# Kernel optimization log

Hardware: AMD Instinct MI355X
Metric: run time of the kernel (lower is better)

## Reference

```python
import jax, jax.numpy as jnp
import numpy as np

B, N, T, D, H, O = 4, 40, 100, 4, 128, 2
E = N * (N - 1)
BN_EPS = 1e-5


def setup_inputs() -> dict:
    ks = jax.random.split(jax.random.key(0), 32)
    def rn(i, shape, s=0.1):
        return jax.random.normal(ks[i], shape, dtype=jnp.float32) * s
    # fully-connected off-diagonal edge list -> one-hot rel matrices (NRI convention)
    off = np.ones((N, N), dtype=np.float32) - np.eye(N, dtype=np.float32)
    r, c = np.where(off > 0)
    eye = np.eye(N, dtype=np.float32)
    return {
        "inputs": jax.random.normal(ks[0], (B, N, T, D), dtype=jnp.float32),
        "rel_rec": jnp.asarray(eye[r]),
        "rel_send": jnp.asarray(eye[c]),
        "conv1_w": rn(1, (H, 2 * D, 5)), "conv1_b": rn(2, (H,)),
        "bn1_g": jnp.ones((H,), jnp.float32), "bn1_b": jnp.zeros((H,), jnp.float32),
        "bn1_m": rn(3, (H,), 0.05), "bn1_v": 1.0 + jnp.abs(rn(4, (H,), 0.05)),
        "conv2_w": rn(5, (H, H, 5)), "conv2_b": rn(6, (H,)),
        "bn2_g": jnp.ones((H,), jnp.float32), "bn2_b": jnp.zeros((H,), jnp.float32),
        "bn2_m": rn(7, (H,), 0.05), "bn2_v": 1.0 + jnp.abs(rn(8, (H,), 0.05)),
        "convp_w": rn(9, (H, H, 1)), "convp_b": rn(10, (H,)),
        "conva_w": rn(11, (1, H, 1)), "conva_b": rn(12, (1,)),
        "mlp1_w1": rn(13, (H, H)), "mlp1_b1": rn(14, (H,)),
        "mlp1_w2": rn(15, (H, H)), "mlp1_b2": rn(16, (H,)),
        "mlp2_w1": rn(17, (H, H)), "mlp2_b1": rn(18, (H,)),
        "mlp2_w2": rn(19, (H, H)), "mlp2_b2": rn(20, (H,)),
        "mlp3_w1": rn(21, (3 * H, H)), "mlp3_b1": rn(22, (H,)),
        "mlp3_w2": rn(23, (H, H)), "mlp3_b2": rn(24, (H,)),
        "fco_w": rn(25, (H, O)), "fco_b": rn(26, (O,)),
    }


def _conv1d(x, w, b):
    # x: [n, Cin, T], w: [Cout, Cin, K] (torch layout), VALID padding, stride 1
    y = jax.lax.conv_general_dilated(x, w, (1,), "VALID", dimension_numbers=("NCH", "OIH", "NCH"))
    return y + b[None, :, None]


def _bn(x, g, b, m, v):
    # eval-mode BatchNorm1d over channel axis 1
    return (x - m[None, :, None]) * jax.lax.rsqrt(v[None, :, None] + BN_EPS) * g[None, :, None] + b[None, :, None]


def _mlp(x, w1, b1, w2, b2):
    # NRI MLP with no_bn=True, dropout off (eval)
    h = jax.nn.elu(x @ w1 + b1)
    return jax.nn.elu(h @ w2 + b2)


def _forward(inputs, rel_rec, rel_send, p):
    # node2edge_temporal: [B,N,T,D] -> [B*E, 2D, T] (senders then receivers)
    xf = inputs.reshape(B, N, T * D)
    recv = jnp.einsum("en,bnf->bef", rel_rec, xf).reshape(B * E, T, D).transpose(0, 2, 1)
    send = jnp.einsum("en,bnf->bef", rel_send, xf).reshape(B * E, T, D).transpose(0, 2, 1)
    x = jnp.concatenate([send, recv], axis=1)
    # CNN over time (eval mode)
    x = _bn(jax.nn.relu(_conv1d(x, p["conv1_w"], p["conv1_b"])), p["bn1_g"], p["bn1_b"], p["bn1_m"], p["bn1_v"])
    n, c, t = x.shape
    x = x.reshape(n, c, t // 2, 2).max(axis=-1)  # MaxPool1d(kernel=2, stride=2)
    x = _bn(jax.nn.relu(_conv1d(x, p["conv2_w"], p["conv2_b"])), p["bn2_g"], p["bn2_b"], p["bn2_m"], p["bn2_v"])
    pred = _conv1d(x, p["convp_w"], p["convp_b"])
    attn = jax.nn.softmax(_conv1d(x, p["conva_w"], p["conva_b"]), axis=2)
    x = (pred * attn).mean(axis=2).reshape(B, E, H)  # attention-weighted temporal pooling
    x = _mlp(x, p["mlp1_w1"], p["mlp1_b1"], p["mlp1_w2"], p["mlp1_b2"])
    x_skip = x
    # edge2node: mean-aggregate incoming edges per node (divide by incoming.size(1)=N)
    inc = jnp.einsum("en,beh->bnh", rel_rec, x) / N
    x = _mlp(inc, p["mlp2_w1"], p["mlp2_b1"], p["mlp2_w2"], p["mlp2_b2"])
    # node2edge: cat(senders, receivers) on feature dim
    sn = jnp.einsum("en,bnh->beh", rel_send, x)
    rc = jnp.einsum("en,bnh->beh", rel_rec, x)
    x = jnp.concatenate([sn, rc, x_skip], axis=2)
    x = _mlp(x, p["mlp3_w1"], p["mlp3_b1"], p["mlp3_w2"], p["mlp3_b2"])
    return x @ p["fco_w"] + p["fco_b"]


def reference(inputs, rel_rec, rel_send, conv1_w, conv1_b, bn1_g, bn1_b, bn1_m, bn1_v, conv2_w, conv2_b, bn2_g, bn2_b, bn2_m, bn2_v, convp_w, convp_b, conva_w, conva_b, mlp1_w1, mlp1_b1, mlp1_w2, mlp1_b2, mlp2_w1, mlp2_b1, mlp2_w2, mlp2_b2, mlp3_w1, mlp3_b1, mlp3_w2, mlp3_b2, fco_w, fco_b):
    args = dict(locals())
    p = {k: v for k, v in args.items() if k not in ("inputs", "rel_rec", "rel_send")}
    return _forward(inputs, rel_rec, rel_send, p)
```

## Files before the change

kernel.cpp:

```cpp
#include <hip/hip_runtime.h>

#define E_CNT 1560
#define B_CNT 4
#define N_CNT 40
#define T_CNT 100

typedef __attribute__((ext_vector_type(8))) short bf16x8;
typedef __attribute__((ext_vector_type(4))) float f32x4;

__device__ __forceinline__ short f2bf(float f) {
  union { float f; unsigned u; } v; v.f = f;
  unsigned r = v.u + 0x7FFFu + ((v.u >> 16) & 1u);
  return (short)(r >> 16);
}
__device__ __forceinline__ float bf2f(short s) {
  union { unsigned u; float f; } v; v.u = ((unsigned)(unsigned short)s) << 16;
  return v.f;
}
__device__ __forceinline__ int cvtpk(float lo, float hi) {
  int r;
  asm("v_cvt_pk_bf16_f32 %0, %1, %2" : "=v"(r) : "v"(lo), "v"(hi));
  return r;
}
__device__ __forceinline__ float eluf(float x) { return x > 0.f ? x : (__expf(x) - 1.f); }
__device__ __forceinline__ f32x4 mfma16(bf16x8 a, bf16x8 b, f32x4 c) {
  return __builtin_amdgcn_mfma_f32_16x16x32_bf16(a, b, c, 0, 0, 0);
}
__device__ __forceinline__ int swz(int row, int bytecol) {
  return row * 256 + (bytecol ^ ((row & 7) << 4));
}

enum : size_t {
  OFF_A1   = 0,
  OFF_A2   = OFF_A1 + 16384,
  OFF_INPB = OFF_A2 + 163840,
  OFF_B1F  = OFF_INPB + 128000,
  OFF_O1   = OFF_B1F + 512,
  OFF_B2F  = OFF_O1 + 512,
  OFF_O2   = OFF_B2F + 512,
  OFF_BC1  = OFF_O2 + 512,
  OFF_W1T1 = OFF_BC1 + 512,
  OFF_W1T2 = OFF_W1T1 + 32768,
  OFF_W3T1 = OFF_W1T2 + 32768,
  OFF_W3T2 = OFF_W3T1 + 98304,
  OFF_RIDX = OFF_W3T2 + 32768,
  OFF_SIDX = OFF_RIDX + 6400,
  OFF_EF   = OFF_SIDX + 6400,
  OFF_XSK  = OFF_EF + 1597440,
  OFF_XN   = OFF_XSK + 1597440,
  WS_NEED  = OFF_XN + 40960
};

__global__ void k_prep(
    const float* __restrict__ inp,
    const float* __restrict__ c1w, const float* __restrict__ c1b,
    const float* __restrict__ c2w, const float* __restrict__ c2b,
    const float* __restrict__ cpw, const float* __restrict__ cpb,
    const float* __restrict__ g1, const float* __restrict__ be1, const float* __restrict__ m1, const float* __restrict__ v1,
    const float* __restrict__ g2, const float* __restrict__ be2, const float* __restrict__ m2, const float* __restrict__ v2,
    const float* __restrict__ m1w1, const float* __restrict__ m1b1, const float* __restrict__ m1w2,
    const float* __restrict__ m3w1, const float* __restrict__ m3w2,
    const float* __restrict__ relr, const float* __restrict__ rels,
    short* __restrict__ A1, short* __restrict__ A2, short* __restrict__ inpb,
    float* __restrict__ b1f, float* __restrict__ o1, float* __restrict__ b2f, float* __restrict__ o2,
    float* __restrict__ bc1,
    short* __restrict__ w1t1, short* __restrict__ w1t2, short* __restrict__ w3t1, short* __restrict__ w3t2,
    int* __restrict__ ridx, int* __restrict__ sidx)
{
  const int id = blockIdx.x * blockDim.x + threadIdx.x;
  const int NTH = gridDim.x * blockDim.x;
  for (int i = id; i < 8192; i += NTH) {
    int co = i >> 6, col = i & 63, k = col >> 3, c = col & 7;
    float sa = g1[co] * rsqrtf(v1[co] + 1e-5f);
    A1[i] = (k < 5) ? f2bf(c1w[co * 40 + c * 5 + k] * sa) : (short)0;
  }
  for (int i = id; i < 81920; i += NTH) {
    int s = i >> 14, rem = i & 16383, co = rem >> 7, ci = rem & 127;
    float sb = g2[co] * rsqrtf(v2[co] + 1e-5f);
    A2[i] = f2bf(c2w[(co * 128 + ci) * 5 + s] * sb);
  }
  for (int i = id; i < 64000; i += NTH) inpb[i] = f2bf(inp[i]);
  for (int i = id; i < 128; i += NTH) {
    float sa = g1[i] * rsqrtf(v1[i] + 1e-5f);
    b1f[i] = c1b[i] * sa; o1[i] = be1[i] - m1[i] * sa;
    float sb = g2[i] * rsqrtf(v2[i] + 1e-5f);
    b2f[i] = c2b[i] * sb; o2[i] = be2[i] - m2[i] * sb;
  }
  for (int idx = id; idx < 16384; idx += NTH) {
    int c = idx >> 7, i = idx & 127;
    float s = 0.f;
    for (int o = 0; o < 128; ++o) s += cpw[o * 128 + i] * m1w1[o * 128 + c];
    w1t1[idx] = f2bf(s);
  }
  for (int c = id; c < 128; c += NTH) {
    float s = 0.f;
    for (int o = 0; o < 128; ++o) s += cpb[o] * m1w1[o * 128 + c];
    bc1[c] = m1b1[c] + s * (1.0f / 44.0f);
  }
  for (int i = id; i < 16384; i += NTH) {
    int co = i >> 7, k = i & 127;
    w1t2[i] = f2bf(m1w2[k * 128 + co]);
    w3t2[i] = f2bf(m3w2[k * 128 + co]);
  }
  for (int i = id; i < 49152; i += NTH) {
    int co = i / 384, k = i - co * 384;
    w3t1[i] = f2bf(m3w1[k * 128 + co]);
  }
  for (int i = id; i < E_CNT; i += NTH) {
    int rr = 0, ss = 0;
    for (int n = 0; n < N_CNT; ++n) {
      if (relr[i * N_CNT + n] > 0.5f) rr = n;
      if (rels[i * N_CNT + n] > 0.5f) ss = n;
    }
    ridx[i] = rr; sidx[i] = ss;
  }
}

__global__ __launch_bounds__(256, 5) void k_cnn(
    const short* __restrict__ inpb,
    const short* __restrict__ A1, const short* __restrict__ A2,
    const float* __restrict__ b1fv, const float* __restrict__ o1v,
    const float* __restrict__ b2fv, const float* __restrict__ o2v,
    const float* __restrict__ wa,
    const int* __restrict__ ridx, const int* __restrict__ sidx,
    short* __restrict__ ef)
{
  __shared__ short h1t[2][52 * 128];
  __shared__ short rawb[4 * 408];
  __shared__ float lgp[2][4][48];
  __shared__ float attnS[2][48];

  const int tid = threadIdx.x;
  const int lane = tid & 63;
  const int w = tid >> 6;
  const int g = lane >> 4;
  const int lr = lane & 15;

  const int eg0 = blockIdx.x * 2;
  const int b = eg0 / E_CNT;
  const int e0 = eg0 - b * E_CNT;
  const short* nbase = inpb + (size_t)b * N_CNT * 400;

  if (tid < 200) {
    int row = tid / 50, off = (tid % 50) * 8;
    int e = row >> 1;
    int node = (row & 1) ? ridx[e0 + e] : sidx[e0 + e];
    *(bf16x8*)&rawb[row * 408 + off] = *(const bf16x8*)(nbase + node * 400 + off);
  }
  {
    int ee = tid >> 7, off = (tid & 127) * 4;
    *(short4*)&h1t[ee][48 * 128 + off] = make_short4(0, 0, 0, 0);
  }
  __syncthreads();

  {
    bf16x8 a1f[2][2];
#pragma unroll
    for (int ks = 0; ks < 2; ++ks)
#pragma unroll
      for (int m = 0; m < 2; ++m)
        a1f[ks][m] = *(const bf16x8*)(A1 + (32 * w + 16 * m + lr) * 64 + ks * 32 + 8 * g);
    f32x4 bc[2], oc[2];
#pragma unroll
    for (int m = 0; m < 2; ++m) {
      int rb = 32 * w + 16 * m + 4 * g;
      bc[m] = *(const f32x4*)(b1fv + rb);
      oc[m] = *(const f32x4*)(o1v + rb);
    }
#pragma unroll
    for (int e = 0; e < 2; ++e) {
#pragma unroll
      for (int n = 0; n < 6; ++n) {
        f32x4 acc[2];
        acc[0] = f32x4{0.f, 0.f, 0.f, 0.f};
        acc[1] = f32x4{0.f, 0.f, 0.f, 0.f};
#pragma unroll
        for (int ks = 0; ks < 2; ++ks) {
          int tc = n * 16 + lr + 4 * ks + g;
          tc = tc > 99 ? 99 : tc;
          union { bf16x8 v; int2 h[2]; } u;
          u.h[0] = *(const int2*)&rawb[(2 * e) * 408 + tc * 4];
          u.h[1] = *(const int2*)&rawb[(2 * e + 1) * 408 + tc * 4];
#pragma unroll
          for (int m = 0; m < 2; ++m) acc[m] = mfma16(a1f[ks][m], u.v, acc[m]);
        }
#pragma unroll
        for (int m = 0; m < 2; ++m) {
          int rb = 32 * w + 16 * m + 4 * g;
          float p[4];
#pragma unroll
          for (int r = 0; r < 4; ++r) {
            float v = fmaxf(acc[m][r] + bc[m][r], 0.f) + oc[m][r];
            float o = __shfl_xor(v, 1);
            p[r] = fmaxf(v, o);
          }
          int lo = cvtpk(p[0], p[1]), hi = cvtpk(p[2], p[3]);
          if ((lane & 1) == 0) {
            int t = 8 * n + (lr >> 1);
            *(int2*)((char*)h1t[e] + swz(t, rb * 2)) = make_int2(lo, hi);
          }
        }
      }
    }
  }
  __syncthreads();

  f32x4 acc[2][2][3];
#pragma unroll
  for (int e = 0; e < 2; ++e)
#pragma unroll
    for (int m = 0; m < 2; ++m)
#pragma unroll
      for (int n = 0; n < 3; ++n) acc[e][m][n] = f32x4{0.f, 0.f, 0.f, 0.f};
  {
    const short* a2b = A2 + (32 * w + lr) * 128 + 8 * g;
    const int c0 = 16 * g;
#pragma unroll
    for (int sh = 0; sh < 5; ++sh) {
      const int rowb = (lr + sh) * 256;
      const int xr = ((lr + sh) & 7) << 4;
#pragma unroll
      for (int ks = 0; ks < 4; ++ks) {
        bf16x8 af0 = *(const bf16x8*)(a2b + sh * 16384 + ks * 32);
        bf16x8 af1 = *(const bf16x8*)(a2b + sh * 16384 + 16 * 128 + ks * 32);
        const char* p0 = (const char*)h1t[0] + (rowb + ((ks * 64 + c0) ^ xr));
#pragma unroll
        for (int e = 0; e < 2; ++e) {
          const char* pe = p0 + e * 13312;
#pragma unroll
          for (int n = 0; n < 3; ++n) {
            bf16x8 bfr = *(const bf16x8*)(pe + n * 4096);
            acc[e][0][n] = mfma16(af0, bfr, acc[e][0][n]);
            acc[e][1][n] = mfma16(af1, bfr, acc[e][1][n]);
          }
        }
      }
    }
  }

  {
    f32x4 bc2[2], oc2[2], wam[2];
#pragma unroll
    for (int m = 0; m < 2; ++m) {
      int rb = 32 * w + 16 * m + 4 * g;
      bc2[m] = *(const f32x4*)(b2fv + rb);
      oc2[m] = *(const f32x4*)(o2v + rb);
      wam[m] = *(const f32x4*)(wa + rb);
    }
#pragma unroll
    for (int e = 0; e < 2; ++e)
#pragma unroll
      for (int n = 0; n < 3; ++n) {
        float p = 0.f;
#pragma unroll
        for (int m = 0; m < 2; ++m) {
#pragma unroll
          for (int r = 0; r < 4; ++r) {
            float v = fmaxf(acc[e][m][n][r] + bc2[m][r], 0.f) + oc2[m][r];
            acc[e][m][n][r] = v;
            p += wam[m][r] * v;
          }
        }
        p += __shfl_xor(p, 16);
        p += __shfl_xor(p, 32);
        if (g == 0) lgp[e][w][n * 16 + lr] = p;
      }
  }
  __syncthreads();

  if (w < 2) {
    int ee = w;
    float x = -3e38f;
    if (lane < 44) x = lgp[ee][0][lane] + lgp[ee][1][lane] + lgp[ee][2][lane] + lgp[ee][3][lane];
    float mx = x;
#pragma unroll
    for (int d = 32; d; d >>= 1) mx = fmaxf(mx, __shfl_xor(mx, d));
    float ex = (lane < 44) ? __expf(x - mx) : 0.f;
    float sm = ex;
#pragma unroll
    for (int d = 32; d; d >>= 1) sm += __shfl_xor(sm, d);
    if (lane < 48) attnS[ee][lane] = (lane < 44) ? ex / (sm * 44.f) : 0.f;
  }
  __syncthreads();

#pragma unroll
  for (int e = 0; e < 2; ++e)
#pragma unroll
    for (int m = 0; m < 2; ++m) {
      f32x4 red = f32x4{0.f, 0.f, 0.f, 0.f};
#pragma unroll
      for (int n = 0; n < 3; ++n) {
        float aw = attnS[e][n * 16 + lr];
        red += acc[e][m][n] * aw;
      }
      float p[4];
#pragma unroll
      for (int r = 0; r < 4; ++r) {
        float q = red[r];
        q += __shfl_xor(q, 1);
        q += __shfl_xor(q, 2);
        q += __shfl_xor(q, 4);
        q += __shfl_xor(q, 8);
        p[r] = q;
      }
      int lo = cvtpk(p[0], p[1]), hi = cvtpk(p[2], p[3]);
      if (lr == 0)
        *(int2*)(ef + (size_t)(eg0 + e) * 128 + 32 * w + 16 * m + 4 * g) = make_int2(lo, hi);
    }
}

__global__ __launch_bounds__(256, 2) void k_mlp1(
    const short* __restrict__ ef,
    const short* __restrict__ w1t, const float* __restrict__ b1,
    const short* __restrict__ w2t, const float* __restrict__ b2,
    short* __restrict__ xskip)
{
  __shared__ short hbuf[16 * 136];
  __shared__ short obuf[16 * 128];
  const int tid = threadIdx.x, lane = tid & 63, w = tid >> 6, g = lane >> 4, lr = lane & 15;
  const int mbase = blockIdx.x * 16;

  f32x4 acc[2];
  acc[0] = f32x4{0.f, 0.f, 0.f, 0.f};
  acc[1] = f32x4{0.f, 0.f, 0.f, 0.f};
#pragma unroll
  for (int ks = 0; ks < 4; ++ks) {
    bf16x8 afr = *(const bf16x8*)(ef + (size_t)(mbase + lr) * 128 + ks * 32 + 8 * g);
#pragma unroll
    for (int ni = 0; ni < 2; ++ni) {
      int co = (2 * w + ni) * 16 + lr;
      bf16x8 bfr = *(const bf16x8*)(w1t + co * 128 + ks * 32 + 8 * g);
      acc[ni] = mfma16(afr, bfr, acc[ni]);
    }
  }
#pragma unroll
  for (int ni = 0; ni < 2; ++ni) {
    int co = (2 * w + ni) * 16 + lr;
    float bias = b1[co];
#pragma unroll
    for (int r = 0; r < 4; ++r) hbuf[(4 * g + r) * 136 + co] = f2bf(eluf(acc[ni][r] + bias));
  }
  __syncthreads();
  acc[0] = f32x4{0.f, 0.f, 0.f, 0.f};
  acc[1] = f32x4{0.f, 0.f, 0.f, 0.f};
#pragma unroll
  for (int ks = 0; ks < 4; ++ks) {
    bf16x8 afr = *(const bf16x8*)&hbuf[lr * 136 + ks * 32 + 8 * g];
#pragma unroll
    for (int ni = 0; ni < 2; ++ni) {
      int co = (2 * w + ni) * 16 + lr;
      bf16x8 bfr = *(const bf16x8*)(w2t + co * 128 + ks * 32 + 8 * g);
      acc[ni] = mfma16(afr, bfr, acc[ni]);
    }
  }
#pragma unroll
  for (int ni = 0; ni < 2; ++ni) {
    int co = (2 * w + ni) * 16 + lr;
    float bias = b2[co];
#pragma unroll
    for (int r = 0; r < 4; ++r) obuf[(4 * g + r) * 128 + co] = f2bf(eluf(acc[ni][r] + bias));
  }
  __syncthreads();
  *(bf16x8*)(xskip + (size_t)mbase * 128 + tid * 8) = *(const bf16x8*)&obuf[tid * 8];
}

__global__ __launch_bounds__(128, 4) void k_node(
    const short* __restrict__ xskip, const int* __restrict__ ridx,
    const float* __restrict__ w1, const float* __restrict__ b1,
    const float* __restrict__ w2, const float* __restrict__ b2,
    short* __restrict__ xn)
{
  __shared__ float incs[128];
  __shared__ float hb[128];
  __shared__ int lst[64];
  __shared__ int lcnt;
  const int tid = threadIdx.x;
  const int bn_ = blockIdx.x;
  const int b = bn_ / N_CNT, n = bn_ - b * N_CNT;
  if (tid == 0) lcnt = 0;
  __syncthreads();
  for (int e2 = tid; e2 < E_CNT; e2 += 128) {
    if (ridx[e2] == n) {
      int p = atomicAdd(&lcnt, 1);
      if (p < 64) lst[p] = e2;
    }
  }
  __syncthreads();
  const int m_ = lcnt < 64 ? lcnt : 64;
  const short* base = xskip + (size_t)b * E_CNT * 128 + tid;
  float acc = 0.f;
  for (int i = 0; i < m_; ++i) acc += bf2f(base[(size_t)lst[i] * 128]);
  incs[tid] = acc * 0.025f;
  __syncthreads();
  float h = b1[tid];
  for (int k = 0; k < 128; ++k) h += incs[k] * w1[k * 128 + tid];
  hb[tid] = eluf(h);
  __syncthreads();
  float h2 = b2[tid];
  for (int k = 0; k < 128; ++k) h2 += hb[k] * w2[k * 128 + tid];
  xn[(size_t)bn_ * 128 + tid] = f2bf(eluf(h2));
}

__global__ __launch_bounds__(256, 2) void k_final(
    const short* __restrict__ xn, const short* __restrict__ xskip,
    const int* __restrict__ ridx, const int* __restrict__ sidx,
    const short* __restrict__ w1t, const float* __restrict__ b1,
    const short* __restrict__ w2t, const float* __restrict__ b2,
    const float* __restrict__ fcw, const float* __restrict__ fcb,
    float* __restrict__ out)
{
  __shared__ short hbuf[16 * 136];
  __shared__ short h2buf[16 * 136];
  const int tid = threadIdx.x, lane = tid & 63, w = tid >> 6, g = lane >> 4, lr = lane & 15;
  const int mbase = blockIdx.x * 16;
  const int row = mbase + lr;
  const int b = row / E_CNT;
  const int e = row - b * E_CNT;
  const short* aS = xn + (size_t)(b * N_CNT + sidx[e]) * 128;
  const short* aR = xn + (size_t)(b * N_CNT + ridx[e]) * 128;
  const short* aK = xskip + (size_t)row * 128;

  f32x4 acc[2];
  acc[0] = f32x4{0.f, 0.f, 0.f, 0.f};
  acc[1] = f32x4{0.f, 0.f, 0.f, 0.f};
#pragma unroll
  for (int ks = 0; ks < 12; ++ks) {
    int k = ks * 32 + 8 * g;
    const short* ap = (k < 128) ? (aS + k) : (k < 256) ? (aR + (k - 128)) : (aK + (k - 256));
    bf16x8 afr = *(const bf16x8*)ap;
#pragma unroll
    for (int ni = 0; ni < 2; ++ni) {
      int co = (2 * w + ni) * 16 + lr;
      bf16x8 bfr = *(const bf16x8*)(w1t + co * 384 + ks * 32 + 8 * g);
      acc[ni] = mfma16(afr, bfr, acc[ni]);
    }
  }
#pragma unroll
  for (int ni = 0; ni < 2; ++ni) {
    int co = (2 * w + ni) * 16 + lr;
    float bias = b1[co];
#pragma unroll
    for (int r = 0; r < 4; ++r) hbuf[(4 * g + r) * 136 + co] = f2bf(eluf(acc[ni][r] + bias));
  }
  __syncthreads();
  acc[0] = f32x4{0.f, 0.f, 0.f, 0.f};
  acc[1] = f32x4{0.f, 0.f, 0.f, 0.f};
#pragma unroll
  for (int ks = 0; ks < 4; ++ks) {
    bf16x8 afr = *(const bf16x8*)&hbuf[lr * 136 + ks * 32 + 8 * g];
#pragma unroll
    for (int ni = 0; ni < 2; ++ni) {
      int co = (2 * w + ni) * 16 + lr;
      bf16x8 bfr = *(const bf16x8*)(w2t + co * 128 + ks * 32 + 8 * g);
      acc[ni] = mfma16(afr, bfr, acc[ni]);
    }
  }
#pragma unroll
  for (int ni = 0; ni < 2; ++ni) {
    int co = (2 * w + ni) * 16 + lr;
    float bias = b2[co];
#pragma unroll
    for (int r = 0; r < 4; ++r) h2buf[(4 * g + r) * 136 + co] = f2bf(eluf(acc[ni][r] + bias));
  }
  __syncthreads();
  if (tid < 32) {
    int e2 = tid >> 1, o = tid & 1;
    float s = fcb[o];
    for (int k = 0; k < 128; ++k) s += bf2f(h2buf[e2 * 136 + k]) * fcw[k * 2 + o];
    out[(size_t)(mbase + e2) * 2 + o] = s;
  }
}

extern "C" void kernel_launch(void* const* d_in, const int* in_sizes, int n_in,
                              void* d_out, int out_size, void* d_ws, size_t ws_size,
                              hipStream_t stream) {
  (void)in_sizes; (void)n_in; (void)out_size; (void)ws_size;
  const float* inp  = (const float*)d_in[0];
  const float* relr = (const float*)d_in[1];
  const float* rels = (const float*)d_in[2];
  const float* c1w  = (const float*)d_in[3];
  const float* c1b  = (const float*)d_in[4];
  const float* g1   = (const float*)d_in[5];
  const float* be1  = (const float*)d_in[6];
  const float* m1   = (const float*)d_in[7];
  const float* v1   = (const float*)d_in[8];
  const float* c2w  = (const float*)d_in[9];
  const float* c2b  = (const float*)d_in[10];
  const float* g2   = (const float*)d_in[11];
  const float* be2  = (const float*)d_in[12];
  const float* m2   = (const float*)d_in[13];
  const float* v2   = (const float*)d_in[14];
  const float* cpw  = (const float*)d_in[15];
  const float* cpb  = (const float*)d_in[16];
  const float* caw  = (const float*)d_in[17];
  const float* m1w1 = (const float*)d_in[19];
  const float* m1b1 = (const float*)d_in[20];
  const float* m1w2 = (const float*)d_in[21];
  const float* m1b2 = (const float*)d_in[22];
  const float* m2w1 = (const float*)d_in[23];
  const float* m2b1 = (const float*)d_in[24];
  const float* m2w2 = (const float*)d_in[25];
  const float* m2b2 = (const float*)d_in[26];
  const float* m3w1 = (const float*)d_in[27];
  const float* m3b1 = (const float*)d_in[28];
  const float* m3w2 = (const float*)d_in[29];
  const float* m3b2 = (const float*)d_in[30];
  const float* fcw  = (const float*)d_in[31];
  const float* fcb  = (const float*)d_in[32];
  float* out = (float*)d_out;

  char* ws = (char*)d_ws;
  short* A1   = (short*)(ws + OFF_A1);
  short* A2   = (short*)(ws + OFF_A2);
  short* inpb = (short*)(ws + OFF_INPB);
  float* b1f  = (float*)(ws + OFF_B1F);
  float* o1   = (float*)(ws + OFF_O1);
  float* b2f  = (float*)(ws + OFF_B2F);
  float* o2   = (float*)(ws + OFF_O2);
  float* bc1  = (float*)(ws + OFF_BC1);
  short* w1t1 = (short*)(ws + OFF_W1T1);
  short* w1t2 = (short*)(ws + OFF_W1T2);
  short* w3t1 = (short*)(ws + OFF_W3T1);
  short* w3t2 = (short*)(ws + OFF_W3T2);
  int*   ridx = (int*)(ws + OFF_RIDX);
  int*   sidx = (int*)(ws + OFF_SIDX);
  short* ef   = (short*)(ws + OFF_EF);
  short* xsk  = (short*)(ws + OFF_XSK);
  short* xn   = (short*)(ws + OFF_XN);

  k_prep<<<256, 256, 0, stream>>>(inp, c1w, c1b, c2w, c2b, cpw, cpb,
                                  g1, be1, m1, v1, g2, be2, m2, v2,
                                  m1w1, m1b1, m1w2, m3w1, m3w2, relr, rels,
                                  A1, A2, inpb, b1f, o1, b2f, o2, bc1,
                                  w1t1, w1t2, w3t1, w3t2, ridx, sidx);
  k_cnn<<<B_CNT * E_CNT / 2, 256, 0, stream>>>(inpb, A1, A2, b1f, o1, b2f, o2,
                                               caw, ridx, sidx, ef);
  k_mlp1<<<390, 256, 0, stream>>>(ef, w1t1, bc1, w1t2, m1b2, xsk);
  k_node<<<B_CNT * N_CNT, 128, 0, stream>>>(xsk, ridx, m2w1, m2b1, m2w2, m2b2, xn);
  k_final<<<390, 256, 0, stream>>>(xn, xsk, ridx, sidx, w3t1, m3b1, w3t2, m3b2, fcw, fcb, out);
}
```

Measured before the change: 127.3 us.

## Split CNN kernel work across 8 waves, one edge per wave group

The CNN kernel now launches 512 threads per block instead of 256, assigning each group of four waves to one of the two edges rather than having every wave loop over both edges. This halves the per-wave accumulator count and the per-wave MFMA chain, which cuts register pressure and adds more waves to hide latency. In exchange, each wave reloads the A1/A2 weight fragments for its own edge, so weight loads per block double. The larger block may also reduce the number of resident blocks per CU.

```diff
diff --git a/kernel.cpp b/kernel.cpp
--- a/kernel.cpp
+++ b/kernel.cpp
@@ -116,7 +116,7 @@
   }
 }
 
-__global__ __launch_bounds__(256, 5) void k_cnn(
+__global__ __launch_bounds__(512, 8) void k_cnn(
     const short* __restrict__ inpb,
     const short* __restrict__ A1, const short* __restrict__ A2,
     const float* __restrict__ b1fv, const float* __restrict__ o1v,
@@ -135,6 +135,8 @@
   const int w = tid >> 6;
   const int g = lane >> 4;
   const int lr = lane & 15;
+  const int e = w >> 2;
+  const int q = w & 3;
 
   const int eg0 = blockIdx.x * 2;
   const int b = eg0 / E_CNT;
@@ -143,14 +145,11 @@
 
   if (tid < 200) {
     int row = tid / 50, off = (tid % 50) * 8;
-    int e = row >> 1;
-    int node = (row & 1) ? ridx[e0 + e] : sidx[e0 + e];
+    int ee = row >> 1;
+    int node = (row & 1) ? ridx[e0 + ee] : sidx[e0 + ee];
     *(bf16x8*)&rawb[row * 408 + off] = *(const bf16x8*)(nbase + node * 400 + off);
   }
-  {
-    int ee = tid >> 7, off = (tid & 127) * 4;
-    *(short4*)&h1t[ee][48 * 128 + off] = make_short4(0, 0, 0, 0);
-  }
+  ((int*)h1t[tid >> 8])[3072 + (tid & 255)] = 0;
   __syncthreads();
 
   {
@@ -159,61 +158,57 @@
     for (int ks = 0; ks < 2; ++ks)
 #pragma unroll
       for (int m = 0; m < 2; ++m)
-        a1f[ks][m] = *(const bf16x8*)(A1 + (32 * w + 16 * m + lr) * 64 + ks * 32 + 8 * g);
+        a1f[ks][m] = *(const bf16x8*)(A1 + (32 * q + 16 * m + lr) * 64 + ks * 32 + 8 * g);
     f32x4 bc[2], oc[2];
 #pragma unroll
     for (int m = 0; m < 2; ++m) {
-      int rb = 32 * w + 16 * m + 4 * g;
+      int rb = 32 * q + 16 * m + 4 * g;
       bc[m] = *(const f32x4*)(b1fv + rb);
       oc[m] = *(const f32x4*)(o1v + rb);
     }
 #pragma unroll
-    for (int e = 0; e < 2; ++e) {
-#pragma unroll
-      for (int n = 0; n < 6; ++n) {
-        f32x4 acc[2];
-        acc[0] = f32x4{0.f, 0.f, 0.f, 0.f};
-        acc[1] = f32x4{0.f, 0.f, 0.f, 0.f};
-#pragma unroll
-        for (int ks = 0; ks < 2; ++ks) {
-          int tc = n * 16 + lr + 4 * ks + g;
-          tc = tc > 99 ? 99 : tc;
-          union { bf16x8 v; int2 h[2]; } u;
-          u.h[0] = *(const int2*)&rawb[(2 * e) * 408 + tc * 4];
-          u.h[1] = *(const int2*)&rawb[(2 * e + 1) * 408 + tc * 4];
-#pragma unroll
-          for (int m = 0; m < 2; ++m) acc[m] = mfma16(a1f[ks][m], u.v, acc[m]);
+    for (int n = 0; n < 6; ++n) {
+      f32x4 acc1[2];
+      acc1[0] = f32x4{0.f, 0.f, 0.f, 0.f};
+      acc1[1] = f32x4{0.f, 0.f, 0.f, 0.f};
+#pragma unroll
+      for (int ks = 0; ks < 2; ++ks) {
+        int tc = n * 16 + lr + 4 * ks + g;
+        tc = tc > 99 ? 99 : tc;
+        union { bf16x8 v; int2 h[2]; } u;
+        u.h[0] = *(const int2*)&rawb[(2 * e) * 408 + tc * 4];
+        u.h[1] = *(const int2*)&rawb[(2 * e + 1) * 408 + tc * 4];
+#pragma unroll
+        for (int m = 0; m < 2; ++m) acc1[m] = mfma16(a1f[ks][m], u.v, acc1[m]);
+      }
+#pragma unroll
+      for (int m = 0; m < 2; ++m) {
+        int rb = 32 * q + 16 * m + 4 * g;
+        float p[4];
+#pragma unroll
+        for (int r = 0; r < 4; ++r) {
+          float v = fmaxf(acc1[m][r] + bc[m][r], 0.f) + oc[m][r];
+          float o = __shfl_xor(v, 1);
+          p[r] = fmaxf(v, o);
         }
-#pragma unroll
-        for (int m = 0; m < 2; ++m) {
-          int rb = 32 * w + 16 * m + 4 * g;
-          float p[4];
-#pragma unroll
-          for (int r = 0; r < 4; ++r) {
-            float v = fmaxf(acc[m][r] + bc[m][r], 0.f) + oc[m][r];
-            float o = __shfl_xor(v, 1);
-            p[r] = fmaxf(v, o);
-          }
-          int lo = cvtpk(p[0], p[1]), hi = cvtpk(p[2], p[3]);
-          if ((lane & 1) == 0) {
-            int t = 8 * n + (lr >> 1);
-            *(int2*)((char*)h1t[e] + swz(t, rb * 2)) = make_int2(lo, hi);
-          }
+        int lo = cvtpk(p[0], p[1]), hi = cvtpk(p[2], p[3]);
+        if ((lane & 1) == 0) {
+          int t = 8 * n + (lr >> 1);
+          *(int2*)((char*)h1t[e] + swz(t, rb * 2)) = make_int2(lo, hi);
         }
       }
     }
   }
   __syncthreads();
 
-  f32x4 acc[2][2][3];
-#pragma unroll
-  for (int e = 0; e < 2; ++e)
-#pragma unroll
-    for (int m = 0; m < 2; ++m)
-#pragma unroll
-      for (int n = 0; n < 3; ++n) acc[e][m][n] = f32x4{0.f, 0.f, 0.f, 0.f};
+  f32x4 acc[2][3];
+#pragma unroll
+  for (int m = 0; m < 2; ++m)
+#pragma unroll
+    for (int n = 0; n < 3; ++n) acc[m][n] = f32x4{0.f, 0.f, 0.f, 0.f};
   {
-    const short* a2b = A2 + (32 * w + lr) * 128 + 8 * g;
+    const short* a2b = A2 + (32 * q + lr) * 128 + 8 * g;
+    const char* hb = (const char*)h1t[e];
     const int c0 = 16 * g;
 #pragma unroll
     for (int sh = 0; sh < 5; ++sh) {
@@ -223,16 +218,12 @@
       for (int ks = 0; ks < 4; ++ks) {
         bf16x8 af0 = *(const bf16x8*)(a2b + sh * 16384 + ks * 32);
         bf16x8 af1 = *(const bf16x8*)(a2b + sh * 16384 + 16 * 128 + ks * 32);
-        const char* p0 = (const char*)h1t[0] + (rowb + ((ks * 64 + c0) ^ xr));
-#pragma unroll
-        for (int e = 0; e < 2; ++e) {
-          const char* pe = p0 + e * 13312;
-#pragma unroll
-          for (int n = 0; n < 3; ++n) {
-            bf16x8 bfr = *(const bf16x8*)(pe + n * 4096);
-            acc[e][0][n] = mfma16(af0, bfr, acc[e][0][n]);
-            acc[e][1][n] = mfma16(af1, bfr, acc[e][1][n]);
-          }
+        const char* p0 = hb + (rowb + ((ks * 64 + c0) ^ xr));
+#pragma unroll
+        for (int n = 0; n < 3; ++n) {
+          bf16x8 bfr = *(const bf16x8*)(p0 + n * 4096);
+          acc[0][n] = mfma16(af0, bfr, acc[0][n]);
+          acc[1][n] = mfma16(af1, bfr, acc[1][n]);
         }
       }
     }
@@ -242,29 +233,27 @@
     f32x4 bc2[2], oc2[2], wam[2];
 #pragma unroll
     for (int m = 0; m < 2; ++m) {
-      int rb = 32 * w + 16 * m + 4 * g;
+      int rb = 32 * q + 16 * m + 4 * g;
       bc2[m] = *(const f32x4*)(b2fv + rb);
       oc2[m] = *(const f32x4*)(o2v + rb);
       wam[m] = *(const f32x4*)(wa + rb);
     }
 #pragma unroll
-    for (int e = 0; e < 2; ++e)
-#pragma unroll
-      for (int n = 0; n < 3; ++n) {
-        float p = 0.f;
-#pragma unroll
-        for (int m = 0; m < 2; ++m) {
-#pragma unroll
-          for (int r = 0; r < 4; ++r) {
-            float v = fmaxf(acc[e][m][n][r] + bc2[m][r], 0.f) + oc2[m][r];
-            acc[e][m][n][r] = v;
-            p += wam[m][r] * v;
-          }
+    for (int n = 0; n < 3; ++n) {
+      float p = 0.f;
+#pragma unroll
+      for (int m = 0; m < 2; ++m) {
+#pragma unroll
+        for (int r = 0; r < 4; ++r) {
+          float v = fmaxf(acc[m][n][r] + bc2[m][r], 0.f) + oc2[m][r];
+          acc[m][n][r] = v;
+          p += wam[m][r] * v;
         }
-        p += __shfl_xor(p, 16);
-        p += __shfl_xor(p, 32);
-        if (g == 0) lgp[e][w][n * 16 + lr] = p;
       }
+      p += __shfl_xor(p, 16);
+      p += __shfl_xor(p, 32);
+      if (g == 0) lgp[e][q][n * 16 + lr] = p;
+    }
   }
   __syncthreads();
 
@@ -284,29 +273,27 @@
   __syncthreads();
 
 #pragma unroll
-  for (int e = 0; e < 2; ++e)
-#pragma unroll
-    for (int m = 0; m < 2; ++m) {
-      f32x4 red = f32x4{0.f, 0.f, 0.f, 0.f};
-#pragma unroll
-      for (int n = 0; n < 3; ++n) {
-        float aw = attnS[e][n * 16 + lr];
-        red += acc[e][m][n] * aw;
-      }
-      float p[4];
-#pragma unroll
-      for (int r = 0; r < 4; ++r) {
-        float q = red[r];
-        q += __shfl_xor(q, 1);
-        q += __shfl_xor(q, 2);
-        q += __shfl_xor(q, 4);
-        q += __shfl_xor(q, 8);
-        p[r] = q;
-      }
-      int lo = cvtpk(p[0], p[1]), hi = cvtpk(p[2], p[3]);
-      if (lr == 0)
-        *(int2*)(ef + (size_t)(eg0 + e) * 128 + 32 * w + 16 * m + 4 * g) = make_int2(lo, hi);
-    }
+  for (int m = 0; m < 2; ++m) {
+    f32x4 red = f32x4{0.f, 0.f, 0.f, 0.f};
+#pragma unroll
+    for (int n = 0; n < 3; ++n) {
+      float aw = attnS[e][n * 16 + lr];
+      red += acc[m][n] * aw;
+    }
+    float p[4];
+#pragma unroll
+    for (int r = 0; r < 4; ++r) {
+      float s = red[r];
+      s += __shfl_xor(s, 1);
+      s += __shfl_xor(s, 2);
+      s += __shfl_xor(s, 4);
+      s += __shfl_xor(s, 8);
+      p[r] = s;
+    }
+    int lo = cvtpk(p[0], p[1]), hi = cvtpk(p[2], p[3]);
+    if (lr == 0)
+      *(int2*)(ef + (size_t)(eg0 + e) * 128 + 32 * q + 16 * m + 4 * g) = make_int2(lo, hi);
+  }
 }
 
 __global__ __launch_bounds__(256, 2) void k_mlp1(
@@ -533,7 +520,7 @@
                                   m1w1, m1b1, m1w2, m3w1, m3w2, relr, rels,
                                   A1, A2, inpb, b1f, o1, b2f, o2, bc1,
                                   w1t1, w1t2, w3t1, w3t2, ridx, sidx);
-  k_cnn<<<B_CNT * E_CNT / 2, 256, 0, stream>>>(inpb, A1, A2, b1f, o1, b2f, o2,
+  k_cnn<<<B_CNT * E_CNT / 2, 512, 0, stream>>>(inpb, A1, A2, b1f, o1, b2f, o2,
                                                caw, ridx, sidx, ef);
   k_mlp1<<<390, 256, 0, stream>>>(ef, w1t1, bc1, w1t2, m1b2, xsk);
   k_node<<<B_CNT * N_CNT, 128, 0, stream>>>(xsk, ridx, m2w1, m2b1, m2w2, m2b2, xn);
```

Measured after the change: 181.6 us. 42.6% more time.

## Fuse edge MLP1 into the CNN kernel epilogue via shared memory

Applied to the files above, without the earlier changes.

Removes the separate k_mlp1 launch. The k_cnn kernel now keeps its pooled edge features in shared memory, reusing the h1t buffer with a swizzled layout, and runs both MLP1 layers in its epilogue. It writes xskip directly, which drops the global ef round trip and one kernel launch. The catch is that each block covers only 2 edges, so every 16-row MFMA tile is mostly padding, and every one of the 3120 blocks now reads both MLP1 weight matrices from cache. It also adds two block-wide barriers per block.

```diff
diff --git a/kernel.cpp b/kernel.cpp
--- a/kernel.cpp
+++ b/kernel.cpp
@@ -123,12 +123,16 @@
     const float* __restrict__ b2fv, const float* __restrict__ o2v,
     const float* __restrict__ wa,
     const int* __restrict__ ridx, const int* __restrict__ sidx,
-    short* __restrict__ ef)
+    const short* __restrict__ w1t, const float* __restrict__ bc1v,
+    const short* __restrict__ w2t, const float* __restrict__ b2v,
+    short* __restrict__ xskip)
 {
   __shared__ short h1t[2][52 * 128];
   __shared__ short rawb[4 * 408];
   __shared__ float lgp[2][4][48];
   __shared__ float attnS[2][48];
+  short* efl = h1t[0];
+  short* hbl = h1t[0] + 8192;
 
   const int tid = threadIdx.x;
   const int lane = tid & 63;
@@ -305,63 +309,62 @@
       }
       int lo = cvtpk(p[0], p[1]), hi = cvtpk(p[2], p[3]);
       if (lr == 0)
-        *(int2*)(ef + (size_t)(eg0 + e) * 128 + 32 * w + 16 * m + 4 * g) = make_int2(lo, hi);
-    }
-}
-
-__global__ __launch_bounds__(256, 2) void k_mlp1(
-    const short* __restrict__ ef,
-    const short* __restrict__ w1t, const float* __restrict__ b1,
-    const short* __restrict__ w2t, const float* __restrict__ b2,
-    short* __restrict__ xskip)
-{
-  __shared__ short hbuf[16 * 136];
-  __shared__ short obuf[16 * 128];
-  const int tid = threadIdx.x, lane = tid & 63, w = tid >> 6, g = lane >> 4, lr = lane & 15;
-  const int mbase = blockIdx.x * 16;
-
-  f32x4 acc[2];
-  acc[0] = f32x4{0.f, 0.f, 0.f, 0.f};
-  acc[1] = f32x4{0.f, 0.f, 0.f, 0.f};
-#pragma unroll
-  for (int ks = 0; ks < 4; ++ks) {
-    bf16x8 afr = *(const bf16x8*)(ef + (size_t)(mbase + lr) * 128 + ks * 32 + 8 * g);
-#pragma unroll
-    for (int ni = 0; ni < 2; ++ni) {
-      int co = (2 * w + ni) * 16 + lr;
-      bf16x8 bfr = *(const bf16x8*)(w1t + co * 128 + ks * 32 + 8 * g);
-      acc[ni] = mfma16(afr, bfr, acc[ni]);
-    }
-  }
-#pragma unroll
-  for (int ni = 0; ni < 2; ++ni) {
-    int co = (2 * w + ni) * 16 + lr;
-    float bias = b1[co];
-#pragma unroll
-    for (int r = 0; r < 4; ++r) hbuf[(4 * g + r) * 136 + co] = f2bf(eluf(acc[ni][r] + bias));
-  }
-  __syncthreads();
-  acc[0] = f32x4{0.f, 0.f, 0.f, 0.f};
-  acc[1] = f32x4{0.f, 0.f, 0.f, 0.f};
-#pragma unroll
-  for (int ks = 0; ks < 4; ++ks) {
-    bf16x8 afr = *(const bf16x8*)&hbuf[lr * 136 + ks * 32 + 8 * g];
-#pragma unroll
-    for (int ni = 0; ni < 2; ++ni) {
-      int co = (2 * w + ni) * 16 + lr;
-      bf16x8 bfr = *(const bf16x8*)(w2t + co * 128 + ks * 32 + 8 * g);
-      acc[ni] = mfma16(afr, bfr, acc[ni]);
-    }
-  }
-#pragma unroll
-  for (int ni = 0; ni < 2; ++ni) {
-    int co = (2 * w + ni) * 16 + lr;
-    float bias = b2[co];
-#pragma unroll
-    for (int r = 0; r < 4; ++r) obuf[(4 * g + r) * 128 + co] = f2bf(eluf(acc[ni][r] + bias));
-  }
-  __syncthreads();
-  *(bf16x8*)(xskip + (size_t)mbase * 128 + tid * 8) = *(const bf16x8*)&obuf[tid * 8];
+        *(int2*)((char*)efl + swz(e, (32 * w + 16 * m + 4 * g) * 2)) = make_int2(lo, hi);
+    }
+  __syncthreads();
+
+  {
+    f32x4 a1[2];
+    a1[0] = f32x4{0.f, 0.f, 0.f, 0.f};
+    a1[1] = f32x4{0.f, 0.f, 0.f, 0.f};
+#pragma unroll
+    for (int ks = 0; ks < 4; ++ks) {
+      bf16x8 afr = *(const bf16x8*)((char*)efl + swz(lr, (ks * 32 + 8 * g) * 2));
+#pragma unroll
+      for (int ni = 0; ni < 2; ++ni) {
+        int co = (2 * w + ni) * 16 + lr;
+        bf16x8 bfr = *(const bf16x8*)(w1t + co * 128 + ks * 32 + 8 * g);
+        a1[ni] = mfma16(afr, bfr, a1[ni]);
+      }
+    }
+    if (g == 0) {
+#pragma unroll
+      for (int ni = 0; ni < 2; ++ni) {
+        int co = (2 * w + ni) * 16 + lr;
+        float bias = bc1v[co];
+#pragma unroll
+        for (int r = 0; r < 2; ++r)
+          *(short*)((char*)hbl + swz(r, co * 2)) = f2bf(eluf(a1[ni][r] + bias));
+      }
+    }
+  }
+  __syncthreads();
+
+  {
+    f32x4 a2[2];
+    a2[0] = f32x4{0.f, 0.f, 0.f, 0.f};
+    a2[1] = f32x4{0.f, 0.f, 0.f, 0.f};
+#pragma unroll
+    for (int ks = 0; ks < 4; ++ks) {
+      bf16x8 afr = *(const bf16x8*)((char*)hbl + swz(lr, (ks * 32 + 8 * g) * 2));
+#pragma unroll
+      for (int ni = 0; ni < 2; ++ni) {
+        int co = (2 * w + ni) * 16 + lr;
+        bf16x8 bfr = *(const bf16x8*)(w2t + co * 128 + ks * 32 + 8 * g);
+        a2[ni] = mfma16(afr, bfr, a2[ni]);
+      }
+    }
+    if (g == 0) {
+#pragma unroll
+      for (int ni = 0; ni < 2; ++ni) {
+        int co = (2 * w + ni) * 16 + lr;
+        float bias = b2v[co];
+#pragma unroll
+        for (int r = 0; r < 2; ++r)
+          xskip[(size_t)(eg0 + r) * 128 + co] = f2bf(eluf(a2[ni][r] + bias));
+      }
+    }
+  }
 }
 
 __global__ __launch_bounds__(128, 4) void k_node(
@@ -524,7 +527,6 @@
   short* w3t2 = (short*)(ws + OFF_W3T2);
   int*   ridx = (int*)(ws + OFF_RIDX);
   int*   sidx = (int*)(ws + OFF_SIDX);
-  short* ef   = (short*)(ws + OFF_EF);
   short* xsk  = (short*)(ws + OFF_XSK);
   short* xn   = (short*)(ws + OFF_XN);
 
@@ -534,8 +536,8 @@
                                   A1, A2, inpb, b1f, o1, b2f, o2, bc1,
                                   w1t1, w1t2, w3t1, w3t2, ridx, sidx);
   k_cnn<<<B_CNT * E_CNT / 2, 256, 0, stream>>>(inpb, A1, A2, b1f, o1, b2f, o2,
-                                               caw, ridx, sidx, ef);
-  k_mlp1<<<390, 256, 0, stream>>>(ef, w1t1, bc1, w1t2, m1b2, xsk);
+                                               caw, ridx, sidx,
+                                               w1t1, bc1, w1t2, m1b2, xsk);
   k_node<<<B_CNT * N_CNT, 128, 0, stream>>>(xsk, ridx, m2w1, m2b1, m2w2, m2b2, xn);
   k_final<<<390, 256, 0, stream>>>(xn, xsk, ridx, sidx, w3t1, m3b1, w3t2, m3b2, fcw, fcb, out);
 }
```

Measured after the change: 138.7 us. +8.9%, slower.
